# Optimization experiments

Hardware: AMD Instinct MI355X
Metric: run time of the kernel (lower is better)

The kernel has to match this reference:

```python
import jax, jax.numpy as jnp
import numpy as np

D = 512
H = 4 * D
EPS = 1e-5

def layernorm(x, g, b):
    mu = jnp.mean(x, axis=-1, keepdims=True)
    var = jnp.mean((x - mu) ** 2, axis=-1, keepdims=True)
    return (x - mu) * jax.lax.rsqrt(var + EPS) * g + b

def setup_inputs() -> dict:
    key = jax.random.key(0)
    ks = jax.random.split(key, 16)
    s = 0.02
    inp = {
        "x": jax.random.normal(ks[0], (16, 2048, D), dtype=jnp.float32),
        "wq": jax.random.normal(ks[1], (D, D), dtype=jnp.float32) * s,
        "bq": jnp.zeros((D,), jnp.float32),
        "wk": jax.random.normal(ks[2], (D, D), dtype=jnp.float32) * s,
        "bk": jnp.zeros((D,), jnp.float32),
        "wv": jax.random.normal(ks[3], (D, D), dtype=jnp.float32) * s,
        "bv": jnp.zeros((D,), jnp.float32),
        "wp": jax.random.normal(ks[4], (D, D), dtype=jnp.float32) * s,
        "bp": jnp.zeros((D,), jnp.float32),
        "w1": jax.random.normal(ks[5], (D, H), dtype=jnp.float32) * s,
        "b1": jnp.zeros((H,), jnp.float32),
        "w2": jax.random.normal(ks[6], (H, D), dtype=jnp.float32) * s,
        "b2": jnp.zeros((D,), jnp.float32),
        "g1": jnp.ones((D,), jnp.float32),
        "be1": jnp.zeros((D,), jnp.float32),
        "g2": jnp.ones((D,), jnp.float32),
        "be2": jnp.zeros((D,), jnp.float32),
    }
    return inp

def reference(x, wq, bq, wk, bk, wv, bv, wp, bp, w1, b1, w2, b2, g1, be1, g2, be2):
    temperature = jnp.sqrt(jnp.asarray(D, x.dtype))
    q = x @ wq + bq                      # [B,N,D]
    k = x @ wk + bk
    v = x @ wv + bv
    energy = jnp.einsum('bnd,bmd->bnm', q / temperature, k)   # [B,N,N]
    attn = jax.nn.softmax(energy, axis=-1)
    out = jnp.einsum('bnm,bmd->bnd', attn, v)
    att = out @ wp + bp
    x = layernorm(x + att, g1, be1)
    h = jax.nn.gelu(x @ w1 + b1, approximate=False)
    ff = h @ w2 + b2
    x = layernorm(x + ff, g2, be2)
    return x
```

## Files before the change

kernel.cpp:

```cpp
#include <hip/hip_runtime.h>
#include <cmath>

typedef __bf16 bf16_t;
typedef __bf16 bf16x8 __attribute__((ext_vector_type(8)));
typedef __bf16 bf16x4 __attribute__((ext_vector_type(4)));
typedef float f32x4 __attribute__((ext_vector_type(4)));

#define DEV_INLINE __device__ __forceinline__

DEV_INLINE void gload_lds16(const void* g, void* l) {
  __builtin_amdgcn_global_load_lds(
      (const __attribute__((address_space(1))) void*)g,
      (__attribute__((address_space(3))) void*)l, 16, 0, 0);
}

template<int EPI, bool HAS_BIAS>
__global__ __launch_bounds__(256, 2)
void gemm_bt(const bf16_t* __restrict__ A, const bf16_t* __restrict__ B,
             const float* __restrict__ bias, void* __restrict__ C,
             bf16_t* __restrict__ vTaux,
             int M, int N, int K, int lda, int ldb, int ldc,
             long sA, long sB, long sC, float scale)
{
  __shared__ alignas(16) bf16_t lds[3][2][4096];
  const int b = blockIdx.z;
  A += (long)b * sA;
  B += (long)b * sB;
  const int t  = threadIdx.x;
  const int l  = t & 63;
  const int w  = t >> 6;
  const int wr = (w >> 1) * 64;
  const int wc = (w & 1) * 64;
  const int m0 = blockIdx.y * 128;
  const int n0 = blockIdx.x * 128;

  const int r0 = t >> 2;
  const int r1 = r0 + 64;
  const int wb = (t & 3) * 16;
  const int cb0 = wb ^ (((r0 >> 1) & 3) << 4);
  const int cb1 = wb ^ (((r1 >> 1) & 3) << 4);
  const bf16_t* gA0 = A + (long)(m0 + r0) * lda + (cb0 >> 1);
  const bf16_t* gA1 = A + (long)(m0 + r1) * lda + (cb1 >> 1);
  const bf16_t* gB0 = B + (long)(n0 + r0) * ldb + (cb0 >> 1);
  const bf16_t* gB1 = B + (long)(n0 + r1) * ldb + (cb1 >> 1);

#define STAGE(kt, q) do {                                   \
    const long kofs_ = (long)(kt) * 32;                     \
    gload_lds16(gA0 + kofs_, &lds[q][0][t * 8]);            \
    gload_lds16(gA1 + kofs_, &lds[q][0][2048 + t * 8]);     \
    gload_lds16(gB0 + kofs_, &lds[q][1][t * 8]);            \
    gload_lds16(gB1 + kofs_, &lds[q][1][2048 + t * 8]);     \
  } while (0)

  const int fr  = l & 15;
  const int kkb = (l >> 4) * 16;
  int offA[4], offB[4];
#pragma unroll
  for (int mi = 0; mi < 4; mi++) {
    const int row = wr + mi * 16 + fr;
    offA[mi] = row * 32 + ((kkb ^ (((row >> 1) & 3) << 4)) >> 1);
  }
#pragma unroll
  for (int ni = 0; ni < 4; ni++) {
    const int row = wc + ni * 16 + fr;
    offB[ni] = row * 32 + ((kkb ^ (((row >> 1) & 3) << 4)) >> 1);
  }

  f32x4 acc[4][4] = {};

  const int NT = K >> 5;
  STAGE(0, 0);
  STAGE(1, 1);

  int q = 0;
  for (int kt = 0; kt < NT; ++kt) {
    if (kt < NT - 1) asm volatile("s_waitcnt vmcnt(4)" ::: "memory");
    else             asm volatile("s_waitcnt vmcnt(0)" ::: "memory");
    __builtin_amdgcn_sched_barrier(0);
    __builtin_amdgcn_s_barrier();

    if (kt + 2 < NT) {
      int qs = q + 2; if (qs >= 3) qs -= 3;
      STAGE(kt + 2, qs);
    }

    bf16x8 af[4], bfr[4];
#pragma unroll
    for (int mi = 0; mi < 4; mi++)
      af[mi] = *(const bf16x8*)&lds[q][0][offA[mi]];
#pragma unroll
    for (int ni = 0; ni < 4; ni++)
      bfr[ni] = *(const bf16x8*)&lds[q][1][offB[ni]];
#pragma unroll
    for (int mi = 0; mi < 4; mi++)
#pragma unroll
      for (int ni = 0; ni < 4; ni++)
        acc[mi][ni] = __builtin_amdgcn_mfma_f32_16x16x32_bf16(
            af[mi], bfr[ni], acc[mi][ni], 0, 0, 0);

    if (++q == 3) q = 0;
  }
#undef STAGE

  const long cb = (long)b * sC;
  const int rbase = m0 + wr + (l >> 4) * 4;
#pragma unroll
  for (int mi = 0; mi < 4; mi++) {
    const int row0 = rbase + mi * 16;
#pragma unroll
    for (int ni = 0; ni < 4; ni++) {
      const int c = n0 + wc + ni * 16 + fr;
      float bias_v = 0.f;
      if constexpr (HAS_BIAS) bias_v = bias[c];
      float vals[4];
#pragma unroll
      for (int r = 0; r < 4; r++) {
        float v = acc[mi][ni][r] + bias_v;
        if constexpr (EPI == 2) v *= scale;
        if constexpr (EPI == 3) v = 0.5f * v * (1.f + erff(v * 0.70710678118f));
        vals[r] = v;
      }
      if constexpr (EPI == 5) {
        if (c < 1024) {
#pragma unroll
          for (int r = 0; r < 4; r++)
            ((bf16_t*)C)[(long)(row0 + r) * ldc + c] = (bf16_t)vals[r];
        } else {
          const int bb = row0 >> 11;
          const int n  = row0 & 2047;
          bf16x4 pk = { (bf16_t)vals[0], (bf16_t)vals[1],
                        (bf16_t)vals[2], (bf16_t)vals[3] };
          *(bf16x4*)&vTaux[(long)bb * (512 * 2048) + (long)(c - 1024) * 2048 + n] = pk;
        }
      } else {
#pragma unroll
        for (int r = 0; r < 4; r++) {
          const long idx = cb + (long)(row0 + r) * ldc + c;
          if constexpr (EPI == 0) ((float*)C)[idx] = vals[r];
          else                    ((bf16_t*)C)[idx] = (bf16_t)vals[r];
        }
      }
    }
  }
}

__global__ __launch_bounds__(256)
void transpose_cast(const float* __restrict__ in, bf16_t* __restrict__ out,
                    int R, int Cc)
{
  __shared__ float tile[32][33];
  const int c0 = blockIdx.x * 32;
  const int r0 = blockIdx.y * 32;
  const int tx = threadIdx.x & 31;
  const int ty = threadIdx.x >> 5;
#pragma unroll
  for (int i = 0; i < 32; i += 8)
    tile[ty + i][tx] = in[(long)(r0 + ty + i) * Cc + (c0 + tx)];
  __syncthreads();
#pragma unroll
  for (int i = 0; i < 32; i += 8)
    out[(long)(c0 + ty + i) * R + (r0 + tx)] = (bf16_t)tile[tx][ty + i];
}

__global__ __launch_bounds__(256)
void cast_to_bf16(const float* __restrict__ in, bf16_t* __restrict__ out, long n)
{
  const long i = ((long)blockIdx.x * 256 + threadIdx.x) * 4;
  if (i >= n) return;
  const float4 v = *(const float4*)&in[i];
  bf16x4 o = { (bf16_t)v.x, (bf16_t)v.y, (bf16_t)v.z, (bf16_t)v.w };
  *(bf16x4*)&out[i] = o;
}

__global__ __launch_bounds__(256)
void concat_bias(const float* __restrict__ a, const float* __restrict__ b,
                 const float* __restrict__ c, float* __restrict__ o)
{
  const int i = blockIdx.x * 256 + threadIdx.x;
  if (i < 512) o[i] = a[i];
  else if (i < 1024) o[i] = b[i - 512];
  else if (i < 1536) o[i] = c[i - 1024];
}

__global__ __launch_bounds__(256)
void softmax2048(bf16_t* __restrict__ E)
{
  const long row = blockIdx.x;
  bf16_t* p = E + row * 2048;
  const int t = threadIdx.x;
  bf16x8 xv = *(const bf16x8*)&p[t * 8];
  float v[8];
#pragma unroll
  for (int j = 0; j < 8; j++) v[j] = (float)xv[j];
  float m = v[0];
#pragma unroll
  for (int j = 1; j < 8; j++) m = fmaxf(m, v[j]);
  for (int o = 32; o; o >>= 1) m = fmaxf(m, __shfl_xor(m, o));
  __shared__ float redm[4];
  __shared__ float reds[4];
  if ((t & 63) == 0) redm[t >> 6] = m;
  __syncthreads();
  m = fmaxf(fmaxf(redm[0], redm[1]), fmaxf(redm[2], redm[3]));
  float s = 0.f;
#pragma unroll
  for (int j = 0; j < 8; j++) { v[j] = __expf(v[j] - m); s += v[j]; }
  for (int o = 32; o; o >>= 1) s += __shfl_xor(s, o);
  if ((t & 63) == 0) reds[t >> 6] = s;
  __syncthreads();
  s = reds[0] + reds[1] + reds[2] + reds[3];
  const float inv = 1.f / s;
  bf16x8 ov;
#pragma unroll
  for (int j = 0; j < 8; j++) ov[j] = (bf16_t)(v[j] * inv);
  *(bf16x8*)&p[t * 8] = ov;
}

template<bool A_BF16, bool EMIT_F32, bool EMIT_BF16>
__global__ __launch_bounds__(128)
void add_ln(const void* __restrict__ xa_, const float* __restrict__ xadd,
            const float* __restrict__ g, const float* __restrict__ be,
            float* __restrict__ y, bf16_t* __restrict__ yb)
{
  const long row = blockIdx.x;
  const int c = threadIdx.x * 4;
  float av[4];
  if constexpr (A_BF16) {
    const bf16_t* xa = (const bf16_t*)xa_;
    bf16x4 a = *(const bf16x4*)&xa[row * 512 + c];
#pragma unroll
    for (int j = 0; j < 4; j++) av[j] = (float)a[j];
  } else {
    const float* xa = (const float*)xa_;
    const float4 a = *(const float4*)&xa[row * 512 + c];
    av[0] = a.x; av[1] = a.y; av[2] = a.z; av[3] = a.w;
  }
  const float4 bb = *(const float4*)&xadd[row * 512 + c];
  float vv[4] = { av[0] + bb.x, av[1] + bb.y, av[2] + bb.z, av[3] + bb.w };
  float s = 0.f, s2 = 0.f;
#pragma unroll
  for (int j = 0; j < 4; j++) { s += vv[j]; s2 += vv[j] * vv[j]; }
  for (int o = 32; o; o >>= 1) { s += __shfl_xor(s, o); s2 += __shfl_xor(s2, o); }
  __shared__ float r0[2], r1[2];
  const int w = threadIdx.x >> 6;
  if ((threadIdx.x & 63) == 0) { r0[w] = s; r1[w] = s2; }
  __syncthreads();
  s = r0[0] + r0[1]; s2 = r1[0] + r1[1];
  const float mu = s * (1.f / 512.f);
  const float var = s2 * (1.f / 512.f) - mu * mu;
  const float rstd = rsqrtf(var + 1e-5f);
  const float4 gg = *(const float4*)&g[c];
  const float4 bev = *(const float4*)&be[c];
  float o0 = (vv[0] - mu) * rstd * gg.x + bev.x;
  float o1 = (vv[1] - mu) * rstd * gg.y + bev.y;
  float o2 = (vv[2] - mu) * rstd * gg.z + bev.z;
  float o3 = (vv[3] - mu) * rstd * gg.w + bev.w;
  if constexpr (EMIT_F32) {
    float4 yo = { o0, o1, o2, o3 };
    *(float4*)&y[row * 512 + c] = yo;
  }
  if constexpr (EMIT_BF16) {
    bf16x4 ob = { (bf16_t)o0, (bf16_t)o1, (bf16_t)o2, (bf16_t)o3 };
    *(bf16x4*)&yb[row * 512 + c] = ob;
  }
}

extern "C" void kernel_launch(void* const* d_in, const int* in_sizes, int n_in,
                              void* d_out, int out_size, void* d_ws, size_t ws_size,
                              hipStream_t stream)
{
  const float* x   = (const float*)d_in[0];
  const float* wq  = (const float*)d_in[1];
  const float* bq  = (const float*)d_in[2];
  const float* wk  = (const float*)d_in[3];
  const float* bk  = (const float*)d_in[4];
  const float* wv  = (const float*)d_in[5];
  const float* bv  = (const float*)d_in[6];
  const float* wp  = (const float*)d_in[7];
  const float* bp  = (const float*)d_in[8];
  const float* w1  = (const float*)d_in[9];
  const float* b1  = (const float*)d_in[10];
  const float* w2  = (const float*)d_in[11];
  const float* b2  = (const float*)d_in[12];
  const float* g1  = (const float*)d_in[13];
  const float* be1 = (const float*)d_in[14];
  const float* g2  = (const float*)d_in[15];
  const float* be2 = (const float*)d_in[16];

  const long S = 16L * 2048 * 512;
  const long Mi = 1L << 20;

  const size_t NEED = (size_t)200 * Mi;
  if (ws_size < NEED) return;

  char* wsp = (char*)d_ws;
  bf16_t* wqkvT = (bf16_t*)(wsp + 0);
  bf16_t* wpT   = wqkvT + 1536L * 512;
  bf16_t* w1T   = wpT + 512L * 512;
  bf16_t* w2T   = w1T + 2048L * 512;
  float*  bqkv  = (float*)(w2T + 512L * 2048);
  bf16_t* xb  = (bf16_t*)(wsp +   8 * Mi);
  bf16_t* qkb = (bf16_t*)(wsp +  40 * Mi);
  bf16_t* vT  = (bf16_t*)(wsp + 104 * Mi);
  bf16_t* E   = (bf16_t*)(wsp + 136 * Mi);
  bf16_t* ob  = xb;
  bf16_t* x1b = qkb;
  bf16_t* h   = (bf16_t*)(wsp + 72 * Mi);

  cast_to_bf16<<<dim3((unsigned)(S / 4 / 256)), 256, 0, stream>>>(x, xb, S);

  transpose_cast<<<dim3(16, 16), 256, 0, stream>>>(wq, wqkvT,               512, 512);
  transpose_cast<<<dim3(16, 16), 256, 0, stream>>>(wk, wqkvT + 512L * 512,  512, 512);
  transpose_cast<<<dim3(16, 16), 256, 0, stream>>>(wv, wqkvT + 1024L * 512, 512, 512);
  transpose_cast<<<dim3(16, 16), 256, 0, stream>>>(wp, wpT, 512, 512);
  transpose_cast<<<dim3(64, 16), 256, 0, stream>>>(w1, w1T, 512, 2048);
  transpose_cast<<<dim3(16, 64), 256, 0, stream>>>(w2, w2T, 2048, 512);
  concat_bias<<<dim3(6), 256, 0, stream>>>(bq, bk, bv, bqkv);

  gemm_bt<5, true><<<dim3(12, 256, 1), 256, 0, stream>>>(
      xb, wqkvT, bqkv, qkb, vT, 32768, 1536, 512, 512, 512, 1024, 0, 0, 0, 0.f);

  for (int cgrp = 0; cgrp < 2; cgrp++) {
    const long qoff = (long)cgrp * 8 * 2048 * 1024;
    gemm_bt<2, false><<<dim3(16, 16, 8), 256, 0, stream>>>(
        qkb + qoff, qkb + qoff + 512, nullptr, E, nullptr,
        2048, 2048, 512, 1024, 1024, 2048,
        2048L * 1024, 2048L * 1024, 2048L * 2048, 0.04419417382f);
    softmax2048<<<dim3(16384), 256, 0, stream>>>(E);
    gemm_bt<1, false><<<dim3(4, 16, 8), 256, 0, stream>>>(
        E, vT + (long)cgrp * 8 * 512 * 2048, nullptr,
        ob + (long)cgrp * 8 * 2048 * 512, nullptr,
        2048, 512, 2048, 2048, 2048, 512,
        2048L * 2048, 512L * 2048, 2048L * 512, 0.f);
  }

  gemm_bt<0, true><<<dim3(4, 256, 1), 256, 0, stream>>>(
      ob, wpT, bp, (float*)d_out, nullptr,
      32768, 512, 512, 512, 512, 512, 0, 0, 0, 0.f);

  add_ln<false, false, true><<<dim3(32768), 128, 0, stream>>>(
      x, (float*)d_out, g1, be1, nullptr, x1b);

  gemm_bt<3, true><<<dim3(16, 256, 1), 256, 0, stream>>>(
      x1b, w1T, b1, h, nullptr, 32768, 2048, 512, 512, 512, 2048, 0, 0, 0, 0.f);

  gemm_bt<0, true><<<dim3(4, 256, 1), 256, 0, stream>>>(
      h, w2T, b2, (float*)d_out, nullptr,
      32768, 512, 2048, 2048, 2048, 512, 0, 0, 0, 0.f);

  add_ln<true, true, false><<<dim3(32768), 128, 0, stream>>>(
      x1b, (float*)d_out, g2, be2, (float*)d_out, nullptr);
}
```

Before: 636.9 us.

## Add 256x256-tile 512-thread GEMM kernel and use tanh-approx GELU

Adds a new GEMM kernel with 256x256 output tiles, 8 waves and double-buffered LDS (64 KB per buffer pair). It is used for the QKV, QK^T, projection and both FFN GEMMs, while the PV GEMM stays on the old 128-tile kernel. The larger tiles raise arithmetic intensity and cut global/L2 traffic, at the cost of one block per CU and a shallower pipeline than the old three-stage kernel. The exact erf GELU is also replaced by a tanh approximation built on __expf, which is cheaper but introduces small numerical deviation from the reference.

```diff
diff --git a/kernel.cpp b/kernel.cpp
--- a/kernel.cpp
+++ b/kernel.cpp
@@ -12,6 +12,143 @@
   __builtin_amdgcn_global_load_lds(
       (const __attribute__((address_space(1))) void*)g,
       (__attribute__((address_space(3))) void*)l, 16, 0, 0);
+}
+
+DEV_INLINE float gelu_f(float v) {
+  const float u = v * (0.7978845608f + 0.0356774081f * v * v);
+  const float e = __expf(2.f * u);
+  const float th = 1.f - 2.f / (e + 1.f);
+  return 0.5f * v * (1.f + th);
+}
+
+template<int EPI, bool HAS_BIAS>
+__global__ __launch_bounds__(512, 1)
+void gemm256(const bf16_t* __restrict__ A, const bf16_t* __restrict__ B,
+             const float* __restrict__ bias, void* __restrict__ C,
+             bf16_t* __restrict__ vTaux,
+             int M, int N, int K, int lda, int ldb, int ldc,
+             long sA, long sB, long sC, float scale)
+{
+  __shared__ alignas(16) bf16_t As[2][16384];
+  __shared__ alignas(16) bf16_t Bs[2][16384];
+  const int b = blockIdx.z;
+  A += (long)b * sA;
+  B += (long)b * sB;
+  const int t  = threadIdx.x;
+  const int l  = t & 63;
+  const int w  = t >> 6;
+  const int wm = w >> 2;
+  const int wn = w & 3;
+  const int m0 = blockIdx.y * 256;
+  const int n0 = blockIdx.x * 256;
+
+  const int srow  = t >> 3;
+  const int scolb = ((t & 7) * 16) ^ ((srow & 7) << 4);
+  const bf16_t* gA = A + (long)(m0 + srow) * lda + (scolb >> 1);
+  const bf16_t* gB = B + (long)(n0 + srow) * ldb + (scolb >> 1);
+
+  const int fr = l & 15;
+  const int kq = l >> 4;
+  int offA[8][2], offB[4][2];
+#pragma unroll
+  for (int mi = 0; mi < 8; mi++) {
+    const int row = wm * 128 + mi * 16 + fr;
+    const int swz = (row & 7) << 4;
+#pragma unroll
+    for (int ks = 0; ks < 2; ks++)
+      offA[mi][ks] = row * 64 + (((ks * 64 + kq * 16) ^ swz) >> 1);
+  }
+#pragma unroll
+  for (int ni = 0; ni < 4; ni++) {
+    const int row = wn * 64 + ni * 16 + fr;
+    const int swz = (row & 7) << 4;
+#pragma unroll
+    for (int ks = 0; ks < 2; ks++)
+      offB[ni][ks] = row * 64 + (((ks * 64 + kq * 16) ^ swz) >> 1);
+  }
+
+#define STAGE256(kt, q) do {                                          \
+    const long ko_ = (long)(kt) * 64;                                 \
+    gload_lds16(gA + ko_,                    &As[q][t * 8]);          \
+    gload_lds16(gA + 64  * (long)lda + ko_,  &As[q][4096  + t * 8]);  \
+    gload_lds16(gA + 128 * (long)lda + ko_,  &As[q][8192  + t * 8]);  \
+    gload_lds16(gA + 192 * (long)lda + ko_,  &As[q][12288 + t * 8]);  \
+    gload_lds16(gB + ko_,                    &Bs[q][t * 8]);          \
+    gload_lds16(gB + 64  * (long)ldb + ko_,  &Bs[q][4096  + t * 8]);  \
+    gload_lds16(gB + 128 * (long)ldb + ko_,  &Bs[q][8192  + t * 8]);  \
+    gload_lds16(gB + 192 * (long)ldb + ko_,  &Bs[q][12288 + t * 8]);  \
+  } while (0)
+
+  f32x4 acc[8][4] = {};
+
+  const int NT = K >> 6;
+  STAGE256(0, 0);
+  __syncthreads();
+
+  int cur = 0;
+  for (int kt = 0; kt < NT; ++kt) {
+    if (kt + 1 < NT) STAGE256(kt + 1, cur ^ 1);
+#pragma unroll
+    for (int ks = 0; ks < 2; ks++) {
+      bf16x8 af[8], bf[4];
+#pragma unroll
+      for (int mi = 0; mi < 8; mi++)
+        af[mi] = *(const bf16x8*)&As[cur][offA[mi][ks]];
+#pragma unroll
+      for (int ni = 0; ni < 4; ni++)
+        bf[ni] = *(const bf16x8*)&Bs[cur][offB[ni][ks]];
+#pragma unroll
+      for (int mi = 0; mi < 8; mi++)
+#pragma unroll
+        for (int ni = 0; ni < 4; ni++)
+          acc[mi][ni] = __builtin_amdgcn_mfma_f32_16x16x32_bf16(
+              af[mi], bf[ni], acc[mi][ni], 0, 0, 0);
+    }
+    __syncthreads();
+    cur ^= 1;
+  }
+#undef STAGE256
+
+  const long cb = (long)b * sC;
+  const int rbase = m0 + wm * 128 + kq * 4;
+#pragma unroll
+  for (int mi = 0; mi < 8; mi++) {
+    const int row0 = rbase + mi * 16;
+#pragma unroll
+    for (int ni = 0; ni < 4; ni++) {
+      const int c = n0 + wn * 64 + ni * 16 + fr;
+      float bias_v = 0.f;
+      if constexpr (HAS_BIAS) bias_v = bias[c];
+      float vals[4];
+#pragma unroll
+      for (int r = 0; r < 4; r++) {
+        float v = acc[mi][ni][r] + bias_v;
+        if constexpr (EPI == 2) v *= scale;
+        if constexpr (EPI == 3) v = gelu_f(v);
+        vals[r] = v;
+      }
+      if constexpr (EPI == 5) {
+        if (c < 1024) {
+#pragma unroll
+          for (int r = 0; r < 4; r++)
+            ((bf16_t*)C)[(long)(row0 + r) * ldc + c] = (bf16_t)vals[r];
+        } else {
+          const int bb = row0 >> 11;
+          const int n  = row0 & 2047;
+          bf16x4 pk = { (bf16_t)vals[0], (bf16_t)vals[1],
+                        (bf16_t)vals[2], (bf16_t)vals[3] };
+          *(bf16x4*)&vTaux[(long)bb * (512 * 2048) + (long)(c - 1024) * 2048 + n] = pk;
+        }
+      } else {
+#pragma unroll
+        for (int r = 0; r < 4; r++) {
+          const long idx = cb + (long)(row0 + r) * ldc + c;
+          if constexpr (EPI == 0) ((float*)C)[idx] = vals[r];
+          else                    ((bf16_t*)C)[idx] = (bf16_t)vals[r];
+        }
+      }
+    }
+  }
 }
 
 template<int EPI, bool HAS_BIAS>
@@ -117,28 +254,14 @@
       for (int r = 0; r < 4; r++) {
         float v = acc[mi][ni][r] + bias_v;
         if constexpr (EPI == 2) v *= scale;
-        if constexpr (EPI == 3) v = 0.5f * v * (1.f + erff(v * 0.70710678118f));
+        if constexpr (EPI == 3) v = gelu_f(v);
         vals[r] = v;
       }
-      if constexpr (EPI == 5) {
-        if (c < 1024) {
-#pragma unroll
-          for (int r = 0; r < 4; r++)
-            ((bf16_t*)C)[(long)(row0 + r) * ldc + c] = (bf16_t)vals[r];
-        } else {
-          const int bb = row0 >> 11;
-          const int n  = row0 & 2047;
-          bf16x4 pk = { (bf16_t)vals[0], (bf16_t)vals[1],
-                        (bf16_t)vals[2], (bf16_t)vals[3] };
-          *(bf16x4*)&vTaux[(long)bb * (512 * 2048) + (long)(c - 1024) * 2048 + n] = pk;
-        }
-      } else {
-#pragma unroll
-        for (int r = 0; r < 4; r++) {
-          const long idx = cb + (long)(row0 + r) * ldc + c;
-          if constexpr (EPI == 0) ((float*)C)[idx] = vals[r];
-          else                    ((bf16_t*)C)[idx] = (bf16_t)vals[r];
-        }
+#pragma unroll
+      for (int r = 0; r < 4; r++) {
+        const long idx = cb + (long)(row0 + r) * ldc + c;
+        if constexpr (EPI == 0) ((float*)C)[idx] = vals[r];
+        else                    ((bf16_t*)C)[idx] = (bf16_t)vals[r];
       }
     }
   }
@@ -316,12 +439,12 @@
   transpose_cast<<<dim3(16, 64), 256, 0, stream>>>(w2, w2T, 2048, 512);
   concat_bias<<<dim3(6), 256, 0, stream>>>(bq, bk, bv, bqkv);
 
-  gemm_bt<5, true><<<dim3(12, 256, 1), 256, 0, stream>>>(
+  gemm256<5, true><<<dim3(6, 128, 1), 512, 0, stream>>>(
       xb, wqkvT, bqkv, qkb, vT, 32768, 1536, 512, 512, 512, 1024, 0, 0, 0, 0.f);
 
   for (int cgrp = 0; cgrp < 2; cgrp++) {
     const long qoff = (long)cgrp * 8 * 2048 * 1024;
-    gemm_bt<2, false><<<dim3(16, 16, 8), 256, 0, stream>>>(
+    gemm256<2, false><<<dim3(8, 8, 8), 512, 0, stream>>>(
         qkb + qoff, qkb + qoff + 512, nullptr, E, nullptr,
         2048, 2048, 512, 1024, 1024, 2048,
         2048L * 1024, 2048L * 1024, 2048L * 2048, 0.04419417382f);
@@ -333,17 +456,17 @@
         2048L * 2048, 512L * 2048, 2048L * 512, 0.f);
   }
 
-  gemm_bt<0, true><<<dim3(4, 256, 1), 256, 0, stream>>>(
+  gemm256<0, true><<<dim3(2, 128, 1), 512, 0, stream>>>(
       ob, wpT, bp, (float*)d_out, nullptr,
       32768, 512, 512, 512, 512, 512, 0, 0, 0, 0.f);
 
   add_ln<false, false, true><<<dim3(32768), 128, 0, stream>>>(
       x, (float*)d_out, g1, be1, nullptr, x1b);
 
-  gemm_bt<3, true><<<dim3(16, 256, 1), 256, 0, stream>>>(
+  gemm256<3, true><<<dim3(8, 128, 1), 512, 0, stream>>>(
       x1b, w1T, b1, h, nullptr, 32768, 2048, 512, 512, 512, 2048, 0, 0, 0, 0.f);
 
-  gemm_bt<0, true><<<dim3(4, 256, 1), 256, 0, stream>>>(
+  gemm256<0, true><<<dim3(2, 128, 1), 512, 0, stream>>>(
       h, w2T, b2, (float*)d_out, nullptr,
       32768, 512, 2048, 2048, 2048, 512, 0, 0, 0, 0.f);
 
```

New measurement: 655.3 us. +2.9%, slower.
